# Kernel tuning notes

Measured on AMD Instinct MI355X. Metric: run time of the kernel, lower is better.

## Reference

```python
import jax, jax.numpy as jnp
import numpy as np

N = 100000      # nodes
E = 1600000     # edges (avg degree 16)
F_IN = 128      # input feature dim (lazy in_channels=-1)
HID = 256       # hidden_channels
OUT = 128       # out_channels
NCLS = 2        # final softmax classes


def _l2norm(x):
    # F.normalize(p=2, dim=-1) with eps clamp, as SAGEConv(normalize=True)
    n = jnp.linalg.norm(x, axis=-1, keepdims=True)
    return x / jnp.maximum(n, 1e-12)


def _sage(x, src, tgt, Wl, bl, Wr, n_nodes):
    # PyG SAGEConv: mean-aggregate source features at targets, then
    # out = lin_l(mean_aggr) + lin_r(x); lin_l has bias, lin_r does not.
    s = jax.ops.segment_sum(x[src], tgt, num_segments=n_nodes)          # [N, F]
    cnt = jax.ops.segment_sum(jnp.ones((src.shape[0],), x.dtype), tgt,
                              num_segments=n_nodes)                     # [N]
    mean = s / jnp.maximum(cnt, 1.0)[:, None]
    out = mean @ Wl.T + bl + x @ Wr.T
    return _l2norm(out)


def setup_inputs() -> dict:
    key = jax.random.key(0)
    ks = jax.random.split(key, 12)

    def glorot(k, o, i):
        lim = float(np.sqrt(6.0 / (o + i)))
        return jax.random.uniform(k, (o, i), jnp.float32, -lim, lim)

    return {
        "x": jax.random.normal(ks[0], (N, F_IN), jnp.float32),
        "edge_index": jax.random.randint(ks[1], (2, E), 0, N, dtype=jnp.int64),
        # conv1: SAGEConv(F_IN -> HID)
        "W1l": glorot(ks[2], HID, F_IN), "b1l": jnp.zeros((HID,), jnp.float32),
        "W1r": glorot(ks[3], HID, F_IN),
        # linear: HID -> OUT
        "Wlin": glorot(ks[4], OUT, HID), "blin": jnp.zeros((OUT,), jnp.float32),
        # conv2: SAGEConv(OUT -> OUT)
        "W2l": glorot(ks[5], OUT, OUT), "b2l": jnp.zeros((OUT,), jnp.float32),
        "W2r": glorot(ks[6], OUT, OUT),
        # linear2: OUT -> 2
        "Wlin2": glorot(ks[7], NCLS, OUT), "blin2": jnp.zeros((NCLS,), jnp.float32),
    }


def reference(x, edge_index, W1l, b1l, W1r, Wlin, blin, W2l, b2l, W2r, Wlin2, blin2):
    src, tgt = edge_index[0], edge_index[1]
    h = _sage(x, src, tgt, W1l, b1l, W1r, N)            # conv1, normalize
    h = jnp.maximum(h @ Wlin.T + blin, 0.0)             # linear + relu
    y = _sage(h, src, tgt, W2l, b2l, W2r, N)            # conv2, normalize
    logits = y @ Wlin2.T + blin2                        # linear2
    probs = jax.nn.softmax(logits, axis=1)
    return probs, y
```

## Files before the change

### kernel.cpp

```cpp
#include <hip/hip_runtime.h>
#include <hip/hip_bf16.h>
#include <hip/hip_fp8.h>

#define NN   100000
#define NE   1600000
#define NBK  196
#define BSH  9
#define EPB  8192
#define CAP  9216

typedef __attribute__((ext_vector_type(8))) short short8;
typedef __attribute__((ext_vector_type(4))) float f32x4;

__device__ __forceinline__ ushort f2bf(float f) {
    union { float f; uint u; } v; v.f = f;
    uint u = v.u;
    return (ushort)((u + 0x7FFFu + ((u >> 16) & 1u)) >> 16);
}
__device__ __forceinline__ float bf2f(uint b) {
    union { uint u; float f; } v; v.u = b << 16;
    return v.f;
}
__device__ __forceinline__ float fp8f(uint byte) {
    __hip_fp8_e4m3 t; t.__x = (__hip_fp8_storage_t)(byte & 0xffu);
    return (float)t;
}
__device__ __forceinline__ uint f2fp8(float f) {
    __hip_fp8_e4m3 t(f);
    return (uint)t.__x;
}
__device__ __forceinline__ int swz(int off) { return off ^ (((off >> 9) & 7) << 4); }

__global__ __launch_bounds__(256) void bucket_hist(const int* __restrict__ tgt,
                                                   int* __restrict__ bcnt) {
    __shared__ int lh[NBK];
    int tid = threadIdx.x;
    for (int i = tid; i < NBK; i += 256) lh[i] = 0;
    __syncthreads();
    int base4 = blockIdx.x * (EPB / 4);
#pragma unroll
    for (int k = 0; k < 8; ++k) {
        int i4 = base4 + k * 256 + tid;
        if (i4 < NE / 4) {
            int4 t = ((const int4*)tgt)[i4];
            atomicAdd(&lh[t.x >> BSH], 1);
            atomicAdd(&lh[t.y >> BSH], 1);
            atomicAdd(&lh[t.z >> BSH], 1);
            atomicAdd(&lh[t.w >> BSH], 1);
        }
    }
    __syncthreads();
    for (int i = tid; i < NBK; i += 256)
        if (lh[i]) atomicAdd(&bcnt[i], lh[i]);
}

__global__ __launch_bounds__(256) void bucket_scan(const int* __restrict__ bcnt,
                                                   int* __restrict__ bbase,
                                                   int* __restrict__ bcursor,
                                                   int* __restrict__ rowstart) {
    int t = threadIdx.x;
    int v = (t < NBK) ? bcnt[t] : 0;
    int lane = t & 63, wid = t >> 6;
    int inc = v;
#pragma unroll
    for (int off = 1; off < 64; off <<= 1) {
        int u = __shfl_up(inc, off);
        if (lane >= off) inc += u;
    }
    __shared__ int ws[4];
    if (lane == 63) ws[wid] = inc;
    __syncthreads();
    int woff = 0;
    for (int w = 0; w < wid; ++w) woff += ws[w];
    int ex = woff + inc - v;
    if (t < NBK) { bbase[t] = ex; bcursor[t] = ex; }
    if (t == NBK) bbase[NBK] = ex;
    if (t == 255) rowstart[NN] = NE;
}

__global__ __launch_bounds__(256) void bucket_scatter(const int* __restrict__ src,
                                                      const int* __restrict__ tgt,
                                                      int* __restrict__ bcursor,
                                                      uint* __restrict__ brec) {
    __shared__ int lh[NBK + 1];
    __shared__ int lcur[NBK];
    __shared__ int lbase[NBK];
    __shared__ uint lrec[EPB];
    __shared__ int ws[4];
    int tid = threadIdx.x;
    for (int i = tid; i < NBK; i += 256) lh[i] = 0;
    __syncthreads();
    int base4 = blockIdx.x * (EPB / 4);
#pragma unroll
    for (int k = 0; k < 8; ++k) {
        int i4 = base4 + k * 256 + tid;
        if (i4 < NE / 4) {
            int4 t = ((const int4*)tgt)[i4];
            atomicAdd(&lh[t.x >> BSH], 1);
            atomicAdd(&lh[t.y >> BSH], 1);
            atomicAdd(&lh[t.z >> BSH], 1);
            atomicAdd(&lh[t.w >> BSH], 1);
        }
    }
    __syncthreads();
    int v = (tid < NBK) ? lh[tid] : 0;
    int lane = tid & 63, wid = tid >> 6;
    int inc = v;
#pragma unroll
    for (int off = 1; off < 64; off <<= 1) {
        int u = __shfl_up(inc, off);
        if (lane >= off) inc += u;
    }
    if (lane == 63) ws[wid] = inc;
    __syncthreads();
    int woff = 0;
    for (int w = 0; w < wid; ++w) woff += ws[w];
    int ex = woff + inc - v;
    int nval = min(EPB, NE - blockIdx.x * EPB);
    if (tid < NBK) {
        lh[tid] = ex;
        lcur[tid] = ex;
        lbase[tid] = v ? atomicAdd(&bcursor[tid], v) : 0;
    }
    if (tid == 0) lh[NBK] = nval;
    __syncthreads();
#pragma unroll
    for (int k = 0; k < 8; ++k) {
        int i4 = base4 + k * 256 + tid;
        if (i4 < NE / 4) {
            int4 t = ((const int4*)tgt)[i4];
            int4 s = ((const int4*)src)[i4];
            int p;
            p = atomicAdd(&lcur[t.x >> BSH], 1); lrec[p] = ((uint)s.x << BSH) | (uint)(t.x & 511);
            p = atomicAdd(&lcur[t.y >> BSH], 1); lrec[p] = ((uint)s.y << BSH) | (uint)(t.y & 511);
            p = atomicAdd(&lcur[t.z >> BSH], 1); lrec[p] = ((uint)s.z << BSH) | (uint)(t.z & 511);
            p = atomicAdd(&lcur[t.w >> BSH], 1); lrec[p] = ((uint)s.w << BSH) | (uint)(t.w & 511);
        }
    }
    __syncthreads();
    for (int i = tid; i < nval; i += 256) {
        int lo = 0, hi = NBK;
        while (hi - lo > 1) { int mid = (lo + hi) >> 1; if (lh[mid] <= i) lo = mid; else hi = mid; }
        brec[lbase[lo] + (i - lh[lo])] = lrec[i];
    }
}

__global__ __launch_bounds__(256) void bucket_to_csr(const uint* __restrict__ brec,
                                                     const int* __restrict__ bbase,
                                                     int* __restrict__ rowstart,
                                                     int* __restrict__ sortedSrc) {
    __shared__ int cnt[512];
    __shared__ int cur[512];
    __shared__ int srt[CAP];
    __shared__ int ws[4];
    int b = blockIdx.x;
    int beg = bbase[b], end = bbase[b + 1];
    int len = end - beg;
    int n0 = b << BSH;
    int ncnt = min(512, NN - n0);
    int tid = threadIdx.x;
    cnt[tid] = 0; cnt[tid + 256] = 0;
    __syncthreads();
    for (int i = beg + tid; i < end; i += 256)
        atomicAdd(&cnt[brec[i] & 511u], 1);
    __syncthreads();
    int c0 = cnt[2 * tid], c1 = cnt[2 * tid + 1];
    int s = c0 + c1;
    int lane = tid & 63, wid = tid >> 6;
    int inc = s;
#pragma unroll
    for (int off = 1; off < 64; off <<= 1) {
        int u = __shfl_up(inc, off);
        if (lane >= off) inc += u;
    }
    if (lane == 63) ws[wid] = inc;
    __syncthreads();
    int woff = 0;
    for (int w = 0; w < wid; ++w) woff += ws[w];
    int ex = woff + inc - s;
    cur[2 * tid] = ex; cur[2 * tid + 1] = ex + c0;
    if (2 * tid < ncnt)     rowstart[n0 + 2 * tid]     = beg + ex;
    if (2 * tid + 1 < ncnt) rowstart[n0 + 2 * tid + 1] = beg + ex + c0;
    __syncthreads();
    if (len <= CAP) {
        for (int i = beg + tid; i < end; i += 256) {
            uint r = brec[i];
            int p = atomicAdd(&cur[r & 511u], 1);
            srt[p] = (int)(r >> BSH);
        }
        __syncthreads();
        for (int i = tid; i < len; i += 256)
            sortedSrc[beg + i] = srt[i];
    } else {
        for (int i = beg + tid; i < end; i += 256) {
            uint r = brec[i];
            int p = atomicAdd(&cur[r & 511u], 1);
            sortedSrc[beg + p] = (int)(r >> BSH);
        }
    }
}

__global__ __launch_bounds__(256) void gather_mean8(const uchar* __restrict__ t8,
                                                    const int* __restrict__ rowstart,
                                                    const int* __restrict__ sortedSrc,
                                                    ushort* __restrict__ mean) {
    int node = blockIdx.x * 4 + (threadIdx.x >> 6);
    if (node >= NN) return;
    int lane = threadIdx.x & 63;
    int q = lane >> 4, l = lane & 15;
    int beg = rowstart[node], end = rowstart[node + 1];
    float a0 = 0.f, a1 = 0.f, a2 = 0.f, a3 = 0.f;
    float a4 = 0.f, a5 = 0.f, a6 = 0.f, a7 = 0.f;
    float b0 = 0.f, b1 = 0.f, b2 = 0.f, b3 = 0.f;
    float b4 = 0.f, b5 = 0.f, b6 = 0.f, b7 = 0.f;
#define ACCA(v) { a0 += fp8f(v.x);       a1 += fp8f(v.x >> 8); \
                  a2 += fp8f(v.x >> 16); a3 += fp8f(v.x >> 24); \
                  a4 += fp8f(v.y);       a5 += fp8f(v.y >> 8); \
                  a6 += fp8f(v.y >> 16); a7 += fp8f(v.y >> 24); }
#define ACCB(v) { b0 += fp8f(v.x);       b1 += fp8f(v.x >> 8); \
                  b2 += fp8f(v.x >> 16); b3 += fp8f(v.x >> 24); \
                  b4 += fp8f(v.y);       b5 += fp8f(v.y >> 8); \
                  b6 += fp8f(v.y >> 16); b7 += fp8f(v.y >> 24); }
    int i = beg + q;
    for (; i + 4 < end; i += 8) {
        int s0 = sortedSrc[i];
        int s1 = sortedSrc[i + 4];
        uint2 v0 = *(const uint2*)&t8[(size_t)s0 * 128 + l * 8];
        uint2 v1 = *(const uint2*)&t8[(size_t)s1 * 128 + l * 8];
        ACCA(v0) ACCB(v1)
    }
    if (i < end) {
        int s0 = sortedSrc[i];
        uint2 v0 = *(const uint2*)&t8[(size_t)s0 * 128 + l * 8];
        ACCA(v0)
    }
#undef ACCA
#undef ACCB
    a0 += b0; a1 += b1; a2 += b2; a3 += b3;
    a4 += b4; a5 += b5; a6 += b6; a7 += b7;
#define CMB(a) a += __shfl_xor(a, 32); a += __shfl_xor(a, 16);
    CMB(a0) CMB(a1) CMB(a2) CMB(a3) CMB(a4) CMB(a5) CMB(a6) CMB(a7)
#undef CMB
    if (lane < 16) {
        float id = 1.0f / fmaxf((float)(end - beg), 1.0f);
        ushort p[8];
        p[0] = f2bf(a0 * id); p[1] = f2bf(a1 * id);
        p[2] = f2bf(a2 * id); p[3] = f2bf(a3 * id);
        p[4] = f2bf(a4 * id); p[5] = f2bf(a5 * id);
        p[6] = f2bf(a6 * id); p[7] = f2bf(a7 * id);
        *(uint4*)&mean[(size_t)node * 128 + l * 8] = *(uint4*)p;
    }
}

__global__ __launch_bounds__(256) void prep_w(const float* __restrict__ W1l,
                                              const float* __restrict__ W1r,
                                              const float* __restrict__ Wlin,
                                              const float* __restrict__ W2l,
                                              const float* __restrict__ W2r,
                                              ushort* __restrict__ Wcat1,
                                              ushort* __restrict__ Wlinb,
                                              ushort* __restrict__ Wcat2) {
    int i = blockIdx.x * 256 + threadIdx.x;
    if (i < 65536) {
        int o = i >> 8, k = i & 255;
        float v = (k < 128) ? W1l[o * 128 + k] : W1r[o * 128 + k - 128];
        Wcat1[i] = f2bf(v);
    } else if (i < 98304) {
        int j = i - 65536;
        Wlinb[j] = f2bf(Wlin[j]);
    } else {
        int j = i - 98304;
        int o = j >> 8, k = j & 255;
        float v = (k < 128) ? W2l[o * 128 + k] : W2r[o * 128 + k - 128];
        Wcat2[j] = f2bf(v);
    }
}

__global__ __launch_bounds__(256) void xcvt(const float* __restrict__ x,
                                            ushort* __restrict__ xbf,
                                            uchar* __restrict__ x8) {
    int i = blockIdx.x * 256 + threadIdx.x;
    float4 v = ((const float4*)x)[i];
    ushort4 p;
    p.x = f2bf(v.x); p.y = f2bf(v.y); p.z = f2bf(v.z); p.w = f2bf(v.w);
    ((ushort4*)xbf)[i] = p;
    uint q = f2fp8(v.x) | (f2fp8(v.y) << 8) | (f2fp8(v.z) << 16) | (f2fp8(v.w) << 24);
    ((uint*)x8)[i] = q;
}

__global__ __launch_bounds__(256) void cvt8(const ushort* __restrict__ hr,
                                            uchar* __restrict__ hr8) {
    int i = blockIdx.x * 256 + threadIdx.x;
    uint4 v = ((const uint4*)hr)[i];
    uint lo = f2fp8(bf2f(v.x & 0xffffu)) | (f2fp8(bf2f(v.x >> 16)) << 8) |
              (f2fp8(bf2f(v.y & 0xffffu)) << 16) | (f2fp8(bf2f(v.y >> 16)) << 24);
    uint hi = f2fp8(bf2f(v.z & 0xffffu)) | (f2fp8(bf2f(v.z >> 16)) << 8) |
              (f2fp8(bf2f(v.w & 0xffffu)) << 16) | (f2fp8(bf2f(v.w >> 16)) << 24);
    uint2 o; o.x = lo; o.y = hi;
    ((uint2*)hr8)[i] = o;
}

__global__ __launch_bounds__(256) void conv1lin_mfma(const ushort* __restrict__ mean,
                                                     const ushort* __restrict__ xbf,
                                                     const ushort* __restrict__ Wcat,
                                                     const float* __restrict__ bias1,
                                                     const ushort* __restrict__ Wlin,
                                                     const float* __restrict__ blin,
                                                     ushort* __restrict__ hr) {
    __shared__ char As[64 * 512];
    __shared__ char Bs[64 * 512];
    int m0 = blockIdx.x * 64;
    int tid = threadIdx.x;
    for (int c = tid; c < 2048; c += 256) {
        int m = c >> 5, kc = c & 31;
        int mm = min(m0 + m, NN - 1);
        uint4 v = (kc < 16) ? *(const uint4*)&mean[(size_t)mm * 128 + kc * 8]
                            : *(const uint4*)&xbf[(size_t)mm * 128 + (kc - 16) * 8];
        *(uint4*)(As + swz(m * 512 + kc * 16)) = v;
    }
    for (int j = tid; j < 2048; j += 256)
        *(uint4*)(Bs + swz((j >> 5) * 512 + (j & 31) * 16)) = *(const uint4*)&Wcat[j * 8];
    __syncthreads();

    int lane = tid & 63, wave = tid >> 6;
    int col = lane & 15, kg = lane >> 4;
    int mym = wave * 16 + col;
    short8 a[8];
#pragma unroll
    for (int ks = 0; ks < 8; ++ks)
        a[ks] = *(const short8*)(As + swz(mym * 512 + (ks * 32 + kg * 8) * 2));
    f32x4 acc[16];
#pragma unroll
    for (int nt = 0; nt < 4; ++nt) {
        f32x4 c = {0.f, 0.f, 0.f, 0.f};
#pragma unroll
        for (int ks = 0; ks < 8; ++ks)
            c = __builtin_amdgcn_mfma_f32_16x16x32_bf16(
                a[ks], *(const short8*)(Bs + swz((nt * 16 + col) * 512 + (ks * 32 + kg * 8) * 2)), c, 0, 0, 0);
        acc[nt] = c;
    }
    for (int ch = 1; ch < 4; ++ch) {
        __syncthreads();
        for (int j = tid; j < 2048; j += 256)
            *(uint4*)(Bs + swz((j >> 5) * 512 + (j & 31) * 16)) =
                *(const uint4*)&Wcat[ch * 16384 + j * 8];
        __syncthreads();
#pragma unroll
        for (int nt = 0; nt < 4; ++nt) {
            f32x4 c = {0.f, 0.f, 0.f, 0.f};
#pragma unroll
            for (int ks = 0; ks < 8; ++ks)
                c = __builtin_amdgcn_mfma_f32_16x16x32_bf16(
                    a[ks], *(const short8*)(Bs + swz((nt * 16 + col) * 512 + (ks * 32 + kg * 8) * 2)), c, 0, 0, 0);
            acc[ch * 4 + nt] = c;
        }
    }
    float ssq[4] = {0.f, 0.f, 0.f, 0.f};
#pragma unroll
    for (int nt = 0; nt < 16; ++nt) {
        float b = bias1[nt * 16 + col];
#pragma unroll
        for (int r = 0; r < 4; ++r) {
            acc[nt][r] += b;
            ssq[r] += acc[nt][r] * acc[nt][r];
        }
    }
#pragma unroll
    for (int off = 1; off < 16; off <<= 1)
#pragma unroll
        for (int r = 0; r < 4; ++r) ssq[r] += __shfl_xor(ssq[r], off);
    float rn[4];
#pragma unroll
    for (int r = 0; r < 4; ++r) rn[r] = 1.0f / fmaxf(sqrtf(ssq[r]), 1e-12f);
#pragma unroll
    for (int r = 0; r < 4; ++r) {
        int rl = wave * 16 + kg * 4 + r;
#pragma unroll
        for (int nt = 0; nt < 16; ++nt)
            *(ushort*)(As + swz(rl * 512 + (nt * 16 + col) * 2)) = f2bf(acc[nt][r] * rn[r]);
    }
    __syncthreads();
    short8 a2[8];
#pragma unroll
    for (int ks = 0; ks < 8; ++ks)
        a2[ks] = *(const short8*)(As + swz(mym * 512 + (ks * 32 + kg * 8) * 2));
    for (int j = tid; j < 2048; j += 256)
        *(uint4*)(Bs + swz((j >> 5) * 512 + (j & 31) * 16)) = *(const uint4*)&Wlin[j * 8];
    __syncthreads();
    f32x4 acc2[8];
#pragma unroll
    for (int nt = 0; nt < 4; ++nt) {
        f32x4 c = {0.f, 0.f, 0.f, 0.f};
#pragma unroll
        for (int ks = 0; ks < 8; ++ks)
            c = __builtin_amdgcn_mfma_f32_16x16x32_bf16(
                a2[ks], *(const short8*)(Bs + swz((nt * 16 + col) * 512 + (ks * 32 + kg * 8) * 2)), c, 0, 0, 0);
        acc2[nt] = c;
    }
    __syncthreads();
    for (int j = tid; j < 2048; j += 256)
        *(uint4*)(Bs + swz((j >> 5) * 512 + (j & 31) * 16)) = *(const uint4*)&Wlin[16384 + j * 8];
    __syncthreads();
#pragma unroll
    for (int nt = 0; nt < 4; ++nt) {
        f32x4 c = {0.f, 0.f, 0.f, 0.f};
#pragma unroll
        for (int ks = 0; ks < 8; ++ks)
            c = __builtin_amdgcn_mfma_f32_16x16x32_bf16(
                a2[ks], *(const short8*)(Bs + swz((nt * 16 + col) * 512 + (ks * 32 + kg * 8) * 2)), c, 0, 0, 0);
        acc2[4 + nt] = c;
    }
#pragma unroll
    for (int r = 0; r < 4; ++r) {
        int node = m0 + wave * 16 + kg * 4 + r;
        if (node < NN) {
#pragma unroll
            for (int nt = 0; nt < 8; ++nt) {
                float vv = acc2[nt][r] + blin[nt * 16 + col];
                hr[(size_t)node * 128 + nt * 16 + col] = f2bf(fmaxf(vv, 0.f));
            }
        }
    }
}

__global__ __launch_bounds__(256) void conv2_mfma(const ushort* __restrict__ mean,
                                                  const ushort* __restrict__ hr,
                                                  const ushort* __restrict__ Wcat,
                                                  const float* __restrict__ bias,
                                                  const float* __restrict__ Wlin2,
                                                  const float* __restrict__ blin2,
                                                  float* __restrict__ probs,
                                                  float* __restrict__ yout) {
    __shared__ char As[64 * 512];
    __shared__ char Bs[64 * 512];
    int m0 = blockIdx.x * 64;
    int tid = threadIdx.x;
    for (int c = tid; c < 2048; c += 256) {
        int m = c >> 5, kc = c & 31;
        int mm = min(m0 + m, NN - 1);
        uint4 v = (kc < 16) ? *(const uint4*)&mean[(size_t)mm * 128 + kc * 8]
                            : *(const uint4*)&hr[(size_t)mm * 128 + (kc - 16) * 8];
        *(uint4*)(As + swz(m * 512 + kc * 16)) = v;
    }
    for (int j = tid; j < 2048; j += 256)
        *(uint4*)(Bs + swz((j >> 5) * 512 + (j & 31) * 16)) = *(const uint4*)&Wcat[j * 8];
    __syncthreads();

    int lane = tid & 63, wave = tid >> 6;
    int col = lane & 15, kg = lane >> 4;
    int mym = wave * 16 + col;
    short8 a[8];
#pragma unroll
    for (int ks = 0; ks < 8; ++ks)
        a[ks] = *(const short8*)(As + swz(mym * 512 + (ks * 32 + kg * 8) * 2));
    f32x4 acc[8];
#pragma unroll
    for (int nt = 0; nt < 4; ++nt) {
        f32x4 c = {0.f, 0.f, 0.f, 0.f};
#pragma unroll
        for (int ks = 0; ks < 8; ++ks)
            c = __builtin_amdgcn_mfma_f32_16x16x32_bf16(
                a[ks], *(const short8*)(Bs + swz((nt * 16 + col) * 512 + (ks * 32 + kg * 8) * 2)), c, 0, 0, 0);
        acc[nt] = c;
    }
    __syncthreads();
    for (int j = tid; j < 2048; j += 256)
        *(uint4*)(Bs + swz((j >> 5) * 512 + (j & 31) * 16)) = *(const uint4*)&Wcat[16384 + j * 8];
    __syncthreads();
#pragma unroll
    for (int nt = 0; nt < 4; ++nt) {
        f32x4 c = {0.f, 0.f, 0.f, 0.f};
#pragma unroll
        for (int ks = 0; ks < 8; ++ks)
            c = __builtin_amdgcn_mfma_f32_16x16x32_bf16(
                a[ks], *(const short8*)(Bs + swz((nt * 16 + col) * 512 + (ks * 32 + kg * 8) * 2)), c, 0, 0, 0);
        acc[4 + nt] = c;
    }
    float ssq[4] = {0.f, 0.f, 0.f, 0.f};
#pragma unroll
    for (int nt = 0; nt < 8; ++nt) {
        float b = bias[nt * 16 + col];
#pragma unroll
        for (int r = 0; r < 4; ++r) {
            acc[nt][r] += b;
            ssq[r] += acc[nt][r] * acc[nt][r];
        }
    }
#pragma unroll
    for (int off = 1; off < 16; off <<= 1)
#pragma unroll
        for (int r = 0; r < 4; ++r) ssq[r] += __shfl_xor(ssq[r], off);
    float rn[4], p0[4] = {0.f,0.f,0.f,0.f}, p1[4] = {0.f,0.f,0.f,0.f};
#pragma unroll
    for (int r = 0; r < 4; ++r) rn[r] = 1.0f / fmaxf(sqrtf(ssq[r]), 1e-12f);
#pragma unroll
    for (int nt = 0; nt < 8; ++nt) {
        float w0 = Wlin2[nt * 16 + col], w1 = Wlin2[128 + nt * 16 + col];
#pragma unroll
        for (int r = 0; r < 4; ++r) {
            float yv = acc[nt][r] * rn[r];
            acc[nt][r] = yv;
            p0[r] += yv * w0;
            p1[r] += yv * w1;
        }
    }
#pragma unroll
    for (int off = 1; off < 16; off <<= 1)
#pragma unroll
        for (int r = 0; r < 4; ++r) { p0[r] += __shfl_xor(p0[r], off); p1[r] += __shfl_xor(p1[r], off); }
#pragma unroll
    for (int r = 0; r < 4; ++r) {
        int node = m0 + wave * 16 + kg * 4 + r;
        if (node < NN) {
#pragma unroll
            for (int nt = 0; nt < 8; ++nt)
                yout[(size_t)node * 128 + nt * 16 + col] = acc[nt][r];
            if (col == 0) {
                float l0 = p0[r] + blin2[0], l1 = p1[r] + blin2[1];
                float mx = fmaxf(l0, l1);
                float e0 = expf(l0 - mx), e1 = expf(l1 - mx);
                float inv = 1.0f / (e0 + e1);
                probs[(size_t)node * 2 + 0] = e0 * inv;
                probs[(size_t)node * 2 + 1] = e1 * inv;
            }
        }
    }
}

extern "C" void kernel_launch(void* const* d_in, const int* in_sizes, int n_in,
                              void* d_out, int out_size, void* d_ws, size_t ws_size,
                              hipStream_t stream) {
    const float* x     = (const float*)d_in[0];
    const int*   ei    = (const int*)d_in[1];
    const int*   src   = ei;
    const int*   tgt   = ei + NE;
    const float* W1l   = (const float*)d_in[2];
    const float* b1l   = (const float*)d_in[3];
    const float* W1r   = (const float*)d_in[4];
    const float* Wlin  = (const float*)d_in[5];
    const float* blin  = (const float*)d_in[6];
    const float* W2l   = (const float*)d_in[7];
    const float* b2l   = (const float*)d_in[8];
    const float* W2r   = (const float*)d_in[9];
    const float* Wlin2 = (const float*)d_in[10];
    const float* blin2 = (const float*)d_in[11];

    float* probs = (float*)d_out;
    float* y     = (float*)d_out + 2 * NN;

    int*    bcnt      = (int*)d_ws;
    int*    bbase     = bcnt + NBK;
    int*    bcursor   = bbase + NBK + 1;
    int*    rowstart  = bcursor + NBK;
    uint*   brec      = (uint*)(rowstart + NN + 1);
    int*    sortedSrc = (int*)(brec + NE);
    ushort* Wcat1     = (ushort*)(sortedSrc + NE);
    ushort* Wlinb     = Wcat1 + 65536;
    ushort* Wcat2     = Wlinb + 32768;
    ushort* xbf       = Wcat2 + 32768;
    ushort* hr        = xbf + (size_t)NN * 128;
    ushort* mean      = hr + (size_t)NN * 128;
    uchar*  x8        = (uchar*)(mean + (size_t)NN * 128);
    uchar*  hr8       = x8 + (size_t)NN * 128;

    const int NEB = (NE + EPB - 1) / EPB;

    hipMemsetAsync(bcnt, 0, sizeof(int) * NBK, stream);

    prep_w<<<512, 256, 0, stream>>>(W1l, W1r, Wlin, W2l, W2r, Wcat1, Wlinb, Wcat2);
    xcvt<<<NN * 32 / 256, 256, 0, stream>>>(x, xbf, x8);

    bucket_hist<<<NEB, 256, 0, stream>>>(tgt, bcnt);
    bucket_scan<<<1, 256, 0, stream>>>(bcnt, bbase, bcursor, rowstart);
    bucket_scatter<<<NEB, 256, 0, stream>>>(src, tgt, bcursor, brec);
    bucket_to_csr<<<NBK, 256, 0, stream>>>(brec, bbase, rowstart, sortedSrc);

    gather_mean8<<<(NN + 3) / 4, 256, 0, stream>>>(x8, rowstart, sortedSrc, mean);
    conv1lin_mfma<<<(NN + 63) / 64, 256, 0, stream>>>(mean, xbf, Wcat1, b1l,
                                                      Wlinb, blin, hr);
    cvt8<<<NN * 128 / 8 / 256, 256, 0, stream>>>(hr, hr8);
    gather_mean8<<<(NN + 3) / 4, 256, 0, stream>>>(hr8, rowstart, sortedSrc, mean);
    conv2_mfma<<<(NN + 63) / 64, 256, 0, stream>>>(mean, hr, Wcat2, b2l,
                                                   Wlin2, blin2, probs, y);
}
```

Measured before the change: 306.5 us.

## Fuse fp8 conversion into conv1 epilogue and halve weight LDS tile

Removes the separate cvt8 kernel by writing the fp8 copy of hr directly from the conv1+linear epilogue. It also halves the shared-memory B tile to 32 rows, loading weights in smaller chunks with more barriers, which lowers LDS use per block and may raise occupancy. The extra barriers and the scattered byte-wide fp8 stores (one per lane per channel) could cost some of the gain.

Result: slower. 317.4 us (+3.6%).

```diff
diff --git a/kernel.cpp b/kernel.cpp
--- a/kernel.cpp
+++ b/kernel.cpp
@@ -288,27 +288,16 @@
     ((uint*)x8)[i] = q;
 }
 
-__global__ __launch_bounds__(256) void cvt8(const ushort* __restrict__ hr,
-                                            uchar* __restrict__ hr8) {
-    int i = blockIdx.x * 256 + threadIdx.x;
-    uint4 v = ((const uint4*)hr)[i];
-    uint lo = f2fp8(bf2f(v.x & 0xffffu)) | (f2fp8(bf2f(v.x >> 16)) << 8) |
-              (f2fp8(bf2f(v.y & 0xffffu)) << 16) | (f2fp8(bf2f(v.y >> 16)) << 24);
-    uint hi = f2fp8(bf2f(v.z & 0xffffu)) | (f2fp8(bf2f(v.z >> 16)) << 8) |
-              (f2fp8(bf2f(v.w & 0xffffu)) << 16) | (f2fp8(bf2f(v.w >> 16)) << 24);
-    uint2 o; o.x = lo; o.y = hi;
-    ((uint2*)hr8)[i] = o;
-}
-
 __global__ __launch_bounds__(256) void conv1lin_mfma(const ushort* __restrict__ mean,
                                                      const ushort* __restrict__ xbf,
                                                      const ushort* __restrict__ Wcat,
                                                      const float* __restrict__ bias1,
                                                      const ushort* __restrict__ Wlin,
                                                      const float* __restrict__ blin,
-                                                     ushort* __restrict__ hr) {
+                                                     ushort* __restrict__ hr,
+                                                     uchar* __restrict__ hr8) {
     __shared__ char As[64 * 512];
-    __shared__ char Bs[64 * 512];
+    __shared__ char Bs[32 * 512];
     int m0 = blockIdx.x * 64;
     int tid = threadIdx.x;
     for (int c = tid; c < 2048; c += 256) {
@@ -318,8 +307,6 @@
                             : *(const uint4*)&xbf[(size_t)mm * 128 + (kc - 16) * 8];
         *(uint4*)(As + swz(m * 512 + kc * 16)) = v;
     }
-    for (int j = tid; j < 2048; j += 256)
-        *(uint4*)(Bs + swz((j >> 5) * 512 + (j & 31) * 16)) = *(const uint4*)&Wcat[j * 8];
     __syncthreads();
 
     int lane = tid & 63, wave = tid >> 6;
@@ -329,40 +316,32 @@
 #pragma unroll
     for (int ks = 0; ks < 8; ++ks)
         a[ks] = *(const short8*)(As + swz(mym * 512 + (ks * 32 + kg * 8) * 2));
+
     f32x4 acc[16];
-#pragma unroll
-    for (int nt = 0; nt < 4; ++nt) {
-        f32x4 c = {0.f, 0.f, 0.f, 0.f};
-#pragma unroll
-        for (int ks = 0; ks < 8; ++ks)
-            c = __builtin_amdgcn_mfma_f32_16x16x32_bf16(
-                a[ks], *(const short8*)(Bs + swz((nt * 16 + col) * 512 + (ks * 32 + kg * 8) * 2)), c, 0, 0, 0);
-        acc[nt] = c;
-    }
-    for (int ch = 1; ch < 4; ++ch) {
+    for (int ch = 0; ch < 8; ++ch) {
+        if (ch) __syncthreads();
+        for (int j = tid; j < 1024; j += 256)
+            *(uint4*)(Bs + swz((j >> 5) * 512 + (j & 31) * 16)) =
+                *(const uint4*)&Wcat[(size_t)(ch * 32 + (j >> 5)) * 256 + (j & 31) * 8];
         __syncthreads();
-        for (int j = tid; j < 2048; j += 256)
-            *(uint4*)(Bs + swz((j >> 5) * 512 + (j & 31) * 16)) =
-                *(const uint4*)&Wcat[ch * 16384 + j * 8];
-        __syncthreads();
-#pragma unroll
-        for (int nt = 0; nt < 4; ++nt) {
+#pragma unroll
+        for (int nt = 0; nt < 2; ++nt) {
             f32x4 c = {0.f, 0.f, 0.f, 0.f};
 #pragma unroll
             for (int ks = 0; ks < 8; ++ks)
                 c = __builtin_amdgcn_mfma_f32_16x16x32_bf16(
                     a[ks], *(const short8*)(Bs + swz((nt * 16 + col) * 512 + (ks * 32 + kg * 8) * 2)), c, 0, 0, 0);
-            acc[ch * 4 + nt] = c;
+            acc[ch * 2 + nt] = c;
         }
     }
     float ssq[4] = {0.f, 0.f, 0.f, 0.f};
 #pragma unroll
-    for (int nt = 0; nt < 16; ++nt) {
-        float b = bias1[nt * 16 + col];
+    for (int i = 0; i < 16; ++i) {
+        float b = bias1[(i >> 1) * 32 + (i & 1) * 16 + col];
 #pragma unroll
         for (int r = 0; r < 4; ++r) {
-            acc[nt][r] += b;
-            ssq[r] += acc[nt][r] * acc[nt][r];
+            acc[i][r] += b;
+            ssq[r] += acc[i][r] * acc[i][r];
         }
     }
 #pragma unroll
@@ -373,51 +352,45 @@
 #pragma unroll
     for (int r = 0; r < 4; ++r) rn[r] = 1.0f / fmaxf(sqrtf(ssq[r]), 1e-12f);
 #pragma unroll
-    for (int r = 0; r < 4; ++r) {
-        int rl = wave * 16 + kg * 4 + r;
-#pragma unroll
-        for (int nt = 0; nt < 16; ++nt)
-            *(ushort*)(As + swz(rl * 512 + (nt * 16 + col) * 2)) = f2bf(acc[nt][r] * rn[r]);
+    for (int i = 0; i < 16; ++i) {
+        int chan = (i >> 1) * 32 + (i & 1) * 16 + col;
+#pragma unroll
+        for (int r = 0; r < 4; ++r)
+            *(ushort*)(As + swz((wave * 16 + kg * 4 + r) * 512 + chan * 2)) = f2bf(acc[i][r] * rn[r]);
     }
     __syncthreads();
     short8 a2[8];
 #pragma unroll
     for (int ks = 0; ks < 8; ++ks)
         a2[ks] = *(const short8*)(As + swz(mym * 512 + (ks * 32 + kg * 8) * 2));
-    for (int j = tid; j < 2048; j += 256)
-        *(uint4*)(Bs + swz((j >> 5) * 512 + (j & 31) * 16)) = *(const uint4*)&Wlin[j * 8];
-    __syncthreads();
     f32x4 acc2[8];
-#pragma unroll
-    for (int nt = 0; nt < 4; ++nt) {
-        f32x4 c = {0.f, 0.f, 0.f, 0.f};
-#pragma unroll
-        for (int ks = 0; ks < 8; ++ks)
-            c = __builtin_amdgcn_mfma_f32_16x16x32_bf16(
-                a2[ks], *(const short8*)(Bs + swz((nt * 16 + col) * 512 + (ks * 32 + kg * 8) * 2)), c, 0, 0, 0);
-        acc2[nt] = c;
-    }
-    __syncthreads();
-    for (int j = tid; j < 2048; j += 256)
-        *(uint4*)(Bs + swz((j >> 5) * 512 + (j & 31) * 16)) = *(const uint4*)&Wlin[16384 + j * 8];
-    __syncthreads();
-#pragma unroll
-    for (int nt = 0; nt < 4; ++nt) {
-        f32x4 c = {0.f, 0.f, 0.f, 0.f};
-#pragma unroll
-        for (int ks = 0; ks < 8; ++ks)
-            c = __builtin_amdgcn_mfma_f32_16x16x32_bf16(
-                a2[ks], *(const short8*)(Bs + swz((nt * 16 + col) * 512 + (ks * 32 + kg * 8) * 2)), c, 0, 0, 0);
-        acc2[4 + nt] = c;
-    }
-#pragma unroll
-    for (int r = 0; r < 4; ++r) {
-        int node = m0 + wave * 16 + kg * 4 + r;
-        if (node < NN) {
-#pragma unroll
-            for (int nt = 0; nt < 8; ++nt) {
-                float vv = acc2[nt][r] + blin[nt * 16 + col];
-                hr[(size_t)node * 128 + nt * 16 + col] = f2bf(fmaxf(vv, 0.f));
+    for (int lc = 0; lc < 4; ++lc) {
+        if (lc) __syncthreads();
+        for (int j = tid; j < 1024; j += 256)
+            *(uint4*)(Bs + swz((j >> 5) * 512 + (j & 31) * 16)) =
+                *(const uint4*)&Wlin[(size_t)(lc * 32 + (j >> 5)) * 256 + (j & 31) * 8];
+        __syncthreads();
+#pragma unroll
+        for (int nt = 0; nt < 2; ++nt) {
+            f32x4 c = {0.f, 0.f, 0.f, 0.f};
+#pragma unroll
+            for (int ks = 0; ks < 8; ++ks)
+                c = __builtin_amdgcn_mfma_f32_16x16x32_bf16(
+                    a2[ks], *(const short8*)(Bs + swz((nt * 16 + col) * 512 + (ks * 32 + kg * 8) * 2)), c, 0, 0, 0);
+            acc2[lc * 2 + nt] = c;
+        }
+    }
+#pragma unroll
+    for (int i = 0; i < 8; ++i) {
+        int chan = (i >> 1) * 32 + (i & 1) * 16 + col;
+        float b = blin[chan];
+#pragma unroll
+        for (int r = 0; r < 4; ++r) {
+            int node = m0 + wave * 16 + kg * 4 + r;
+            if (node < NN) {
+                float v = fmaxf(acc2[i][r] + b, 0.f);
+                hr[(size_t)node * 128 + chan] = f2bf(v);
+                hr8[(size_t)node * 128 + chan] = (uchar)f2fp8(v);
             }
         }
     }
@@ -432,7 +405,7 @@
                                                   float* __restrict__ probs,
                                                   float* __restrict__ yout) {
     __shared__ char As[64 * 512];
-    __shared__ char Bs[64 * 512];
+    __shared__ char Bs[32 * 512];
     int m0 = blockIdx.x * 64;
     int tid = threadIdx.x;
     for (int c = tid; c < 2048; c += 256) {
@@ -442,8 +415,6 @@
                             : *(const uint4*)&hr[(size_t)mm * 128 + (kc - 16) * 8];
         *(uint4*)(As + swz(m * 512 + kc * 16)) = v;
     }
-    for (int j = tid; j < 2048; j += 256)
-        *(uint4*)(Bs + swz((j >> 5) * 512 + (j & 31) * 16)) = *(const uint4*)&Wcat[j * 8];
     __syncthreads();
 
     int lane = tid & 63, wave = tid >> 6;
@@ -453,37 +424,32 @@
 #pragma unroll
     for (int ks = 0; ks < 8; ++ks)
         a[ks] = *(const short8*)(As + swz(mym * 512 + (ks * 32 + kg * 8) * 2));
+
     f32x4 acc[8];
-#pragma unroll
-    for (int nt = 0; nt < 4; ++nt) {
-        f32x4 c = {0.f, 0.f, 0.f, 0.f};
-#pragma unroll
-        for (int ks = 0; ks < 8; ++ks)
-            c = __builtin_amdgcn_mfma_f32_16x16x32_bf16(
-                a[ks], *(const short8*)(Bs + swz((nt * 16 + col) * 512 + (ks * 32 + kg * 8) * 2)), c, 0, 0, 0);
-        acc[nt] = c;
-    }
-    __syncthreads();
-    for (int j = tid; j < 2048; j += 256)
-        *(uint4*)(Bs + swz((j >> 5) * 512 + (j & 31) * 16)) = *(const uint4*)&Wcat[16384 + j * 8];
-    __syncthreads();
-#pragma unroll
-    for (int nt = 0; nt < 4; ++nt) {
-        f32x4 c = {0.f, 0.f, 0.f, 0.f};
-#pragma unroll
-        for (int ks = 0; ks < 8; ++ks)
-            c = __builtin_amdgcn_mfma_f32_16x16x32_bf16(
-                a[ks], *(const short8*)(Bs + swz((nt * 16 + col) * 512 + (ks * 32 + kg * 8) * 2)), c, 0, 0, 0);
-        acc[4 + nt] = c;
+    for (int ch = 0; ch < 4; ++ch) {
+        if (ch) __syncthreads();
+        for (int j = tid; j < 1024; j += 256)
+            *(uint4*)(Bs + swz((j >> 5) * 512 + (j & 31) * 16)) =
+                *(const uint4*)&Wcat[(size_t)(ch * 32 + (j >> 5)) * 256 + (j & 31) * 8];
+        __syncthreads();
+#pragma unroll
+        for (int nt = 0; nt < 2; ++nt) {
+            f32x4 c = {0.f, 0.f, 0.f, 0.f};
+#pragma unroll
+            for (int ks = 0; ks < 8; ++ks)
+                c = __builtin_amdgcn_mfma_f32_16x16x32_bf16(
+                    a[ks], *(const short8*)(Bs + swz((nt * 16 + col) * 512 + (ks * 32 + kg * 8) * 2)), c, 0, 0, 0);
+            acc[ch * 2 + nt] = c;
+        }
     }
     float ssq[4] = {0.f, 0.f, 0.f, 0.f};
 #pragma unroll
-    for (int nt = 0; nt < 8; ++nt) {
-        float b = bias[nt * 16 + col];
+    for (int i = 0; i < 8; ++i) {
+        float b = bias[(i >> 1) * 32 + (i & 1) * 16 + col];
 #pragma unroll
         for (int r = 0; r < 4; ++r) {
-            acc[nt][r] += b;
-            ssq[r] += acc[nt][r] * acc[nt][r];
+            acc[i][r] += b;
+            ssq[r] += acc[i][r] * acc[i][r];
         }
     }
 #pragma unroll
@@ -494,12 +460,13 @@
 #pragma unroll
     for (int r = 0; r < 4; ++r) rn[r] = 1.0f / fmaxf(sqrtf(ssq[r]), 1e-12f);
 #pragma unroll
-    for (int nt = 0; nt < 8; ++nt) {
-        float w0 = Wlin2[nt * 16 + col], w1 = Wlin2[128 + nt * 16 + col];
+    for (int i = 0; i < 8; ++i) {
+        int chan = (i >> 1) * 32 + (i & 1) * 16 + col;
+        float w0 = Wlin2[chan], w1 = Wlin2[128 + chan];
 #pragma unroll
         for (int r = 0; r < 4; ++r) {
-            float yv = acc[nt][r] * rn[r];
-            acc[nt][r] = yv;
+            float yv = acc[i][r] * rn[r];
+            acc[i][r] = yv;
             p0[r] += yv * w0;
             p1[r] += yv * w1;
         }
@@ -513,8 +480,10 @@
         int node = m0 + wave * 16 + kg * 4 + r;
         if (node < NN) {
 #pragma unroll
-            for (int nt = 0; nt < 8; ++nt)
-                yout[(size_t)node * 128 + nt * 16 + col] = acc[nt][r];
+            for (int i = 0; i < 8; ++i) {
+                int chan = (i >> 1) * 32 + (i & 1) * 16 + col;
+                yout[(size_t)node * 128 + chan] = acc[i][r];
+            }
             if (col == 0) {
                 float l0 = p0[r] + blin2[0], l1 = p1[r] + blin2[1];
                 float mx = fmaxf(l0, l1);
@@ -577,8 +546,7 @@
 
     gather_mean8<<<(NN + 3) / 4, 256, 0, stream>>>(x8, rowstart, sortedSrc, mean);
     conv1lin_mfma<<<(NN + 63) / 64, 256, 0, stream>>>(mean, xbf, Wcat1, b1l,
-                                                      Wlinb, blin, hr);
-    cvt8<<<NN * 128 / 8 / 256, 256, 0, stream>>>(hr, hr8);
+                                                      Wlinb, blin, hr, hr8);
     gather_mean8<<<(NN + 3) / 4, 256, 0, stream>>>(hr8, rowstart, sortedSrc, mean);
     conv2_mfma<<<(NN + 63) / 64, 256, 0, stream>>>(mean, hr, Wcat2, b2l,
                                                    Wlin2, blin2, probs, y);
```
